# Optimization experiments

Hardware: AMD Instinct MI355X
Metric: run time of the kernel (lower is better)

Reference implementation:

```python
import jax, jax.numpy as jnp
import numpy as np

NUM_LABELS = 65  # labels 0..64; 0 is background, 1..64 are instance ids
H, W = 2048, 2048


def setup_inputs() -> dict:
    key = jax.random.key(0)
    k1, k2 = jax.random.split(key)
    pred_mask = jax.random.randint(k1, (H, W), 0, NUM_LABELS, dtype=jnp.int32)
    true_mask = jax.random.randint(k2, (H, W), 0, NUM_LABELS, dtype=jnp.int32)
    return {"pred_mask": pred_mask, "true_mask": true_mask}


def reference(pred_mask, true_mask):
    """Symmetric mean (1 - best IoU) over pred and true instances.

    Replaces the original O(N*M*H*W) nested mask scans with one O(H*W)
    co-occurrence histogram pass + tiny [L,L] vectorized IoU.
    """
    L = NUM_LABELS
    p = pred_mask.reshape(-1).astype(jnp.int32)
    t = true_mask.reshape(-1).astype(jnp.int32)
    # Confusion histogram: conf[i, j] = #pixels with pred==i and true==j
    flat_idx = p * L + t
    conf = jax.ops.segment_sum(
        jnp.ones_like(flat_idx, dtype=jnp.float32), flat_idx,
        num_segments=L * L).reshape(L, L)
    area_pred = conf.sum(axis=1)  # [L] pixels per pred label (incl. bg overlap)
    area_true = conf.sum(axis=0)  # [L]
    # Drop background (label 0) instances, as torch.unique filter does
    inter = conf[1:, 1:]                                   # [L-1, L-1]
    union = area_pred[1:, None] + area_true[None, 1:] - inter
    iou = jnp.where(union > 0, inter / jnp.maximum(union, 1.0), 0.0)
    # Only labels actually present count as instances (torch.unique semantics)
    present_pred = area_pred[1:] > 0
    present_true = area_true[1:] > 0
    # Absent labels have zero intersection everywhere -> iou 0, never best match
    best_for_pred = iou.max(axis=1)  # max over true instances
    best_for_true = iou.max(axis=0)  # max over pred instances
    total = (jnp.sum(jnp.where(present_pred, 1.0 - best_for_pred, 0.0))
             + jnp.sum(jnp.where(present_true, 1.0 - best_for_true, 0.0)))
    n_inst = present_pred.sum() + present_true.sum()
    return jnp.where(n_inst > 0,
                     total / jnp.maximum(n_inst, 1).astype(jnp.float32),
                     jnp.float32(0.0))
```

## Files before the change

### kernel.cpp

```cpp
#include <hip/hip_runtime.h>

#define L 65
#define BINS (L * L)

__global__ void hist_kernel(const int* __restrict__ pred,
                            const int* __restrict__ truem,
                            unsigned int* __restrict__ block_hist,
                            int n, int n4) {
    __shared__ unsigned int sh[BINS];
    for (int i = threadIdx.x; i < BINS; i += blockDim.x) sh[i] = 0u;
    __syncthreads();

    const int4* p4 = (const int4*)pred;
    const int4* t4 = (const int4*)truem;
    int stride = gridDim.x * blockDim.x;
    int gtid = blockIdx.x * blockDim.x + threadIdx.x;

    for (int i = gtid; i < n4; i += stride) {
        int4 p = p4[i];
        int4 t = t4[i];
        atomicAdd(&sh[p.x * L + t.x], 1u);
        atomicAdd(&sh[p.y * L + t.y], 1u);
        atomicAdd(&sh[p.z * L + t.z], 1u);
        atomicAdd(&sh[p.w * L + t.w], 1u);
    }
    for (int i = n4 * 4 + gtid; i < n; i += stride) {
        atomicAdd(&sh[pred[i] * L + truem[i]], 1u);
    }
    __syncthreads();

    unsigned int* dst = block_hist + (size_t)blockIdx.x * BINS;
    for (int i = threadIdx.x; i < BINS; i += blockDim.x) dst[i] = sh[i];
}

__global__ void reduce_kernel(const unsigned int* __restrict__ block_hist,
                              float* __restrict__ conf, int nb) {
    int bin = blockIdx.x * blockDim.x + threadIdx.x;
    if (bin >= BINS) return;
    unsigned int s = 0u;
    for (int b = 0; b < nb; ++b) s += block_hist[(size_t)b * BINS + bin];
    conf[bin] = (float)s;
}

__global__ void finalize_kernel(const float* __restrict__ confg,
                                float* __restrict__ out) {
    __shared__ float conf[BINS];
    __shared__ float area_p[L];
    __shared__ float area_t[L];
    __shared__ float contrib[256];
    __shared__ float cnt[256];
    int tid = threadIdx.x;

    for (int i = tid; i < BINS; i += 256) conf[i] = confg[i];
    __syncthreads();

    if (tid < L) {
        float s = 0.f;
        for (int t = 0; t < L; ++t) s += conf[tid * L + t];
        area_p[tid] = s;
    }
    if (tid >= 128 && tid < 128 + L) {
        int t = tid - 128;
        float s = 0.f;
        for (int p = 0; p < L; ++p) s += conf[p * L + t];
        area_t[t] = s;
    }
    __syncthreads();

    float c = 0.f, k = 0.f;
    if (tid >= 1 && tid < L) {
        int p = tid;
        if (area_p[p] > 0.f) {
            float ap = area_p[p];
            float best = 0.f;
            for (int t = 1; t < L; ++t) {
                float inter = conf[p * L + t];
                float uni = ap + area_t[t] - inter;
                float iou = (uni > 0.f) ? inter / fmaxf(uni, 1.f) : 0.f;
                best = fmaxf(best, iou);
            }
            c = 1.f - best;
            k = 1.f;
        }
    }
    if (tid >= 129 && tid < 128 + L) {
        int t = tid - 128;
        if (area_t[t] > 0.f) {
            float at = area_t[t];
            float best = 0.f;
            for (int p = 1; p < L; ++p) {
                float inter = conf[p * L + t];
                float uni = area_p[p] + at - inter;
                float iou = (uni > 0.f) ? inter / fmaxf(uni, 1.f) : 0.f;
                best = fmaxf(best, iou);
            }
            c = 1.f - best;
            k = 1.f;
        }
    }
    contrib[tid] = c;
    cnt[tid] = k;
    __syncthreads();

    for (int s = 128; s > 0; s >>= 1) {
        if (tid < s) {
            contrib[tid] += contrib[tid + s];
            cnt[tid] += cnt[tid + s];
        }
        __syncthreads();
    }
    if (tid == 0) {
        float n_inst = cnt[0];
        out[0] = (n_inst > 0.f) ? (contrib[0] / fmaxf(n_inst, 1.f)) : 0.f;
    }
}

extern "C" void kernel_launch(void* const* d_in, const int* in_sizes, int n_in,
                              void* d_out, int out_size, void* d_ws, size_t ws_size,
                              hipStream_t stream) {
    const int* pred = (const int*)d_in[0];
    const int* truem = (const int*)d_in[1];
    float* out = (float*)d_out;
    int n = in_sizes[0];
    int n4 = n >> 2;

    size_t per_hist = (size_t)BINS * sizeof(unsigned int);
    int NB = 256;
    size_t need = (size_t)NB * per_hist + BINS * sizeof(float);
    while (NB > 1 && need > ws_size) {
        NB >>= 1;
        need = (size_t)NB * per_hist + BINS * sizeof(float);
    }
    unsigned int* block_hist = (unsigned int*)d_ws;
    float* conf = (float*)((char*)d_ws + (size_t)NB * per_hist);

    hist_kernel<<<NB, 256, 0, stream>>>(pred, truem, block_hist, n, n4);
    reduce_kernel<<<(BINS + 255) / 256, 256, 0, stream>>>(block_hist, conf, NB);
    finalize_kernel<<<1, 256, 0, stream>>>(conf, out);
}
```

Baseline: 119.6 us.

## Enlarge histogram grid and split cross-block reduction into parallel chunks

The histogram kernel now launches 512 blocks of 1024 threads instead of 256 blocks of 256, so more threads stream the inputs and share each block's shared-memory histogram. The reduction over per-block histograms is split across 8 chunks along a second grid dimension, giving 17x8 blocks instead of 17. The finalize kernel then sums the 8 float partials while loading the confusion matrix. More threads per block raise atomic contention on the shared histogram, and partials are summed as floats rather than integers.

```diff
diff --git a/kernel.cpp b/kernel.cpp
--- a/kernel.cpp
+++ b/kernel.cpp
@@ -2,11 +2,12 @@
 
 #define L 65
 #define BINS (L * L)
+#define NCHUNK 8
 
-__global__ void hist_kernel(const int* __restrict__ pred,
-                            const int* __restrict__ truem,
-                            unsigned int* __restrict__ block_hist,
-                            int n, int n4) {
+__global__ __launch_bounds__(1024) void hist_kernel(const int* __restrict__ pred,
+                                                    const int* __restrict__ truem,
+                                                    unsigned int* __restrict__ block_hist,
+                                                    int n, int n4) {
     __shared__ unsigned int sh[BINS];
     for (int i = threadIdx.x; i < BINS; i += blockDim.x) sh[i] = 0u;
     __syncthreads();
@@ -34,15 +35,20 @@
 }
 
 __global__ void reduce_kernel(const unsigned int* __restrict__ block_hist,
-                              float* __restrict__ conf, int nb) {
+                              float* __restrict__ partial,
+                              int nb, int rows_per_chunk) {
     int bin = blockIdx.x * blockDim.x + threadIdx.x;
     if (bin >= BINS) return;
+    int c = blockIdx.y;
+    int r0 = c * rows_per_chunk;
+    int r1 = r0 + rows_per_chunk;
+    if (r1 > nb) r1 = nb;
     unsigned int s = 0u;
-    for (int b = 0; b < nb; ++b) s += block_hist[(size_t)b * BINS + bin];
-    conf[bin] = (float)s;
+    for (int r = r0; r < r1; ++r) s += block_hist[(size_t)r * BINS + bin];
+    partial[(size_t)c * BINS + bin] = (float)s;
 }
 
-__global__ void finalize_kernel(const float* __restrict__ confg,
+__global__ void finalize_kernel(const float* __restrict__ partial,
                                 float* __restrict__ out) {
     __shared__ float conf[BINS];
     __shared__ float area_p[L];
@@ -51,7 +57,12 @@
     __shared__ float cnt[256];
     int tid = threadIdx.x;
 
-    for (int i = tid; i < BINS; i += 256) conf[i] = confg[i];
+    for (int i = tid; i < BINS; i += 256) {
+        float s = 0.f;
+        #pragma unroll
+        for (int c = 0; c < NCHUNK; ++c) s += partial[(size_t)c * BINS + i];
+        conf[i] = s;
+    }
     __syncthreads();
 
     if (tid < L) {
@@ -125,16 +136,21 @@
     int n4 = n >> 2;
 
     size_t per_hist = (size_t)BINS * sizeof(unsigned int);
-    int NB = 256;
-    size_t need = (size_t)NB * per_hist + BINS * sizeof(float);
+    int NB = 512;
+    size_t need = (size_t)NB * per_hist + (size_t)NCHUNK * BINS * sizeof(float);
     while (NB > 1 && need > ws_size) {
         NB >>= 1;
-        need = (size_t)NB * per_hist + BINS * sizeof(float);
+        need = (size_t)NB * per_hist + (size_t)NCHUNK * BINS * sizeof(float);
     }
     unsigned int* block_hist = (unsigned int*)d_ws;
-    float* conf = (float*)((char*)d_ws + (size_t)NB * per_hist);
+    float* partial = (float*)((char*)d_ws + (size_t)NB * per_hist);
 
-    hist_kernel<<<NB, 256, 0, stream>>>(pred, truem, block_hist, n, n4);
-    reduce_kernel<<<(BINS + 255) / 256, 256, 0, stream>>>(block_hist, conf, NB);
-    finalize_kernel<<<1, 256, 0, stream>>>(conf, out);
+    int rows_per_chunk = (NB + NCHUNK - 1) / NCHUNK;
+
+    hist_kernel<<<NB, 1024, 0, stream>>>(pred, truem, block_hist, n, n4);
+
+    dim3 rgrid((BINS + 255) / 256, NCHUNK);
+    reduce_kernel<<<rgrid, 256, 0, stream>>>(block_hist, partial, NB, rows_per_chunk);
+
+    finalize_kernel<<<1, 256, 0, stream>>>(partial, out);
 }
```

Result: faster. 95.91 us (-19.8%).
